# Optimization experiments

Hardware: AMD Instinct MI355X
Metric: run time of the kernel (lower is better)

Reference implementation:

```python
import jax, jax.numpy as jnp
import numpy as np

N = 100_000      # nodes
E = 3_200_000    # edges (avg degree 32)
F_IN, H, C = 1433, 16, 7


def setup_inputs() -> dict:
    key = jax.random.key(0)
    ks = jax.random.split(key, 8)
    x = jax.random.normal(ks[0], (N, F_IN), jnp.float32)
    edge_index = jax.random.randint(ks[1], (2, E), 0, N, dtype=jnp.int32)
    s_in = 1.0 / np.sqrt(F_IN)
    s_h = 1.0 / np.sqrt(H)
    w_root1 = jax.random.normal(ks[2], (F_IN, H), jnp.float32) * s_in
    w_rel1 = jax.random.normal(ks[3], (F_IN, H), jnp.float32) * s_in
    b_rel1 = jnp.zeros((H,), jnp.float32)
    w_root2 = jax.random.normal(ks[4], (H, C), jnp.float32) * s_h
    w_rel2 = jax.random.normal(ks[5], (H, C), jnp.float32) * s_h
    b_rel2 = jnp.zeros((C,), jnp.float32)
    return {"x": x, "edge_index": edge_index,
            "w_root1": w_root1, "w_rel1": w_rel1, "b_rel1": b_rel1,
            "w_root2": w_root2, "w_rel2": w_rel2, "b_rel2": b_rel2}


def _graph_conv(x, src, dst, w_root, w_rel, b_rel, n_nodes):
    # GraphConv: out_i = W_root x_i + W_rel * sum_{j->i} x_j + b.
    # Sum-aggregation commutes with the linear map, so project first
    # (avoids gathering full-width features per edge).
    h = x @ w_rel                                   # [N, out]
    agg = jax.ops.segment_sum(h[src], dst, num_segments=n_nodes)  # [N, out]
    return agg + b_rel + x @ w_root


def reference(x, edge_index, w_root1, w_rel1, b_rel1, w_root2, w_rel2, b_rel2):
    src, dst = edge_index[0], edge_index[1]
    h1 = jax.nn.elu(_graph_conv(x, src, dst, w_root1, w_rel1, b_rel1, N))
    # F.dropout(training=self.training) -> identity in eval mode
    h2 = _graph_conv(h1, src, dst, w_root2, w_rel2, b_rel2, N)
    return jax.nn.log_softmax(h2, axis=1)
```

## Files before the change

### kernel.cpp

```cpp
#include <hip/hip_runtime.h>
#include <hip/hip_bf16.h>
#include <math.h>

#define FIN  1433
#define HID  16
#define NCLS 7
#define BM   128
#define BK   32
#define KS   4
#define KT_TOTAL 45
#define KPAD (KT_TOTAL * BK)

typedef __attribute__((ext_vector_type(8))) short bf16x8;
typedef __attribute__((ext_vector_type(4))) float f32x4;

__global__ __launch_bounds__(256) void k_wt(
    const float* __restrict__ w_root, const float* __restrict__ w_rel,
    ushort* __restrict__ wT) {
  int idx = blockIdx.x * 256 + threadIdx.x;
  if (idx >= 32 * KPAD) return;
  int c = idx / KPAD, k = idx % KPAD;
  float v = 0.f;
  if (k < FIN) v = (c < HID) ? w_rel[k * HID + c] : w_root[k * HID + (c - HID)];
  __hip_bfloat16 h = __float2bfloat16(v);
  wT[idx] = *(ushort*)&h;
}

__global__ __launch_bounds__(256) void k1_mfma(
    const float* __restrict__ x, const ushort* __restrict__ wT,
    const float* __restrict__ b_rel,
    float* __restrict__ pbase, float* __restrict__ abase,
    size_t seg, int n) {
  __shared__ ushort xs[2][BM * BK];
  __shared__ ushort wsh[2][32 * BK];

  const int tid  = threadIdx.x;
  const int lane = tid & 63;
  const int wave = tid >> 6;
  const int row0 = blockIdx.x * BM;
  const int slice = blockIdx.y;
  const int kt_beg = (KT_TOTAL * slice) / KS;
  const int kt_end = (KT_TOTAL * (slice + 1)) / KS;

  f32x4 acc[2][2] = {};

  const int sr  = tid >> 5;
  const int sk  = tid & 31;
  const int wc  = tid >> 3;
  const int wt4 = tid & 7;

  float  xr[16];
  ushort4 wr;

  auto load_tile = [&](int kt) {
    const int k0 = kt * BK;
    const int gk = k0 + sk;
    const bool kv = gk < FIN;
#pragma unroll
    for (int i = 0; i < 16; ++i) {
      int gr = row0 + i * 8 + sr;
      xr[i] = (gr < n && kv) ? x[(size_t)gr * FIN + gk] : 0.f;
    }
    wr = *(const ushort4*)&wT[(size_t)wc * KPAD + k0 + wt4 * 4];
  };

  auto store_stage = [&](int b) {
#pragma unroll
    for (int i = 0; i < 16; ++i) {
      __hip_bfloat16 h = __float2bfloat16(xr[i]);
      xs[b][(i * 8 + sr) * BK + sk] = *(ushort*)&h;
    }
    *(ushort4*)&wsh[b][wc * BK + wt4 * 4] = wr;
  };

  const int m = lane & 15, o = lane >> 4;

  auto do_mfma = [&](int b) {
    bf16x8 b0 = *(const bf16x8*)&wsh[b][(m)      * BK + o * 8];
    bf16x8 b1 = *(const bf16x8*)&wsh[b][(16 + m) * BK + o * 8];
#pragma unroll
    for (int mf = 0; mf < 2; ++mf) {
      bf16x8 a = *(const bf16x8*)&xs[b][(wave * 32 + mf * 16 + m) * BK + o * 8];
      acc[mf][0] = __builtin_amdgcn_mfma_f32_16x16x32_bf16(a, b0, acc[mf][0], 0, 0, 0);
      acc[mf][1] = __builtin_amdgcn_mfma_f32_16x16x32_bf16(a, b1, acc[mf][1], 0, 0, 0);
    }
  };

  load_tile(kt_beg);
  store_stage(0);
  __syncthreads();
  for (int t = kt_beg; t < kt_end; ++t) {
    const int b = (t - kt_beg) & 1;
    const bool more = (t + 1) < kt_end;
    if (more) load_tile(t + 1);
    do_mfma(b);
    if (more) store_stage(b ^ 1);
    __syncthreads();
  }

  float* __restrict__ p_out = pbase + (size_t)slice * seg;
  float* __restrict__ a_out = abase + (size_t)slice * seg;
  const float bv = (slice == 0) ? b_rel[m] : 0.f;
#pragma unroll
  for (int mf = 0; mf < 2; ++mf) {
#pragma unroll
    for (int j = 0; j < 4; ++j) {
      int gr = row0 + wave * 32 + mf * 16 + o * 4 + j;
      if (gr < n) {
        p_out[(size_t)gr * HID + m] = acc[mf][0][j];
        a_out[(size_t)gr * HID + m] = acc[mf][1][j] + bv;
      }
    }
  }
}

__global__ __launch_bounds__(256) void k_reduce(
    float* __restrict__ pbase, float* __restrict__ abase,
    size_t seg_elems, int n4) {
  int i = blockIdx.x * 256 + threadIdx.x;
  if (i >= n4) return;
  size_t s4 = seg_elems / 4;
  float4 a = ((const float4*)pbase)[i];
  float4 c = ((const float4*)abase)[i];
#pragma unroll
  for (int s = 1; s < KS; ++s) {
    float4 b = ((const float4*)pbase)[i + s * s4];
    float4 d = ((const float4*)abase)[i + s * s4];
    a.x += b.x; a.y += b.y; a.z += b.z; a.w += b.w;
    c.x += d.x; c.y += d.y; c.z += d.z; c.w += d.w;
  }
  ((float4*)pbase)[i] = a;
  ((float4*)abase)[i] = c;
}

__global__ __launch_bounds__(256) void k2_scatter16(
    const int* __restrict__ ei, const float* __restrict__ p,
    float* __restrict__ agg, int nE) {
  long long tid = (long long)blockIdx.x * 256 + threadIdx.x;
  if (tid >= (long long)nE * HID) return;
  int e = (int)(tid >> 4), f = (int)(tid & 15);
  int s = ei[e], d = ei[nE + e];
  unsafeAtomicAdd(agg + (size_t)d * HID + f, p[(size_t)s * HID + f]);
}

__global__ __launch_bounds__(256) void k3_l2(
    const float* __restrict__ agg,
    const float* __restrict__ w_root2, const float* __restrict__ w_rel2,
    const float* __restrict__ b2,
    float* __restrict__ p2, float* __restrict__ out2, int n) {
  int i = blockIdx.x * 256 + threadIdx.x;
  if (i >= n) return;
  const float4* a4 = (const float4*)(agg + (size_t)i * HID);
  float h[HID];
#pragma unroll
  for (int q = 0; q < 4; ++q) {
    float4 v = a4[q];
    float t[4] = {v.x, v.y, v.z, v.w};
#pragma unroll
    for (int j = 0; j < 4; ++j)
      h[4*q + j] = t[j] > 0.f ? t[j] : expm1f(t[j]);
  }
#pragma unroll
  for (int c = 0; c < NCLS; ++c) {
    float sr = 0.f, so = b2[c];
#pragma unroll
    for (int k = 0; k < HID; ++k) {
      sr = fmaf(h[k], w_rel2[k * NCLS + c], sr);
      so = fmaf(h[k], w_root2[k * NCLS + c], so);
    }
    p2[(size_t)i * NCLS + c] = sr;
    out2[(size_t)i * NCLS + c] = so;
  }
}

__global__ __launch_bounds__(256) void k4_scatter7(
    const int* __restrict__ ei, const float* __restrict__ p,
    float* __restrict__ out2, int nE) {
  long long tid = (long long)blockIdx.x * 256 + threadIdx.x;
  int e = (int)(tid >> 3), f = (int)(tid & 7);
  if (e >= nE || f >= NCLS) return;
  int s = ei[e], d = ei[nE + e];
  unsafeAtomicAdd(out2 + (size_t)d * NCLS + f, p[(size_t)s * NCLS + f]);
}

__global__ __launch_bounds__(256) void k5_lsm(float* __restrict__ out, int n) {
  int i = blockIdx.x * 256 + threadIdx.x;
  if (i >= n) return;
  float v[NCLS];
  float* o = out + (size_t)i * NCLS;
#pragma unroll
  for (int c = 0; c < NCLS; ++c) v[c] = o[c];
  float m = v[0];
#pragma unroll
  for (int c = 1; c < NCLS; ++c) m = fmaxf(m, v[c]);
  float s = 0.f;
#pragma unroll
  for (int c = 0; c < NCLS; ++c) s += expf(v[c] - m);
  float l = logf(s);
#pragma unroll
  for (int c = 0; c < NCLS; ++c) o[c] = v[c] - m - l;
}

extern "C" void kernel_launch(void* const* d_in, const int* in_sizes, int n_in,
                              void* d_out, int out_size, void* d_ws, size_t ws_size,
                              hipStream_t stream) {
  const float* x       = (const float*)d_in[0];
  const int*   ei      = (const int*)  d_in[1];
  const float* w_root1 = (const float*)d_in[2];
  const float* w_rel1  = (const float*)d_in[3];
  const float* b_rel1  = (const float*)d_in[4];
  const float* w_root2 = (const float*)d_in[5];
  const float* w_rel2  = (const float*)d_in[6];
  const float* b_rel2  = (const float*)d_in[7];
  float* out = (float*)d_out;

  int n  = in_sizes[0] / FIN;
  int nE = in_sizes[1] / 2;

  size_t seg = (size_t)n * HID;
  char* ws = (char*)d_ws;
  float*  pbase = (float*)ws;
  float*  abase = pbase + KS * seg;
  float*  p2    = abase + KS * seg;
  ushort* wT    = (ushort*)(p2 + (size_t)n * NCLS);

  int nbN = (n + 255) / 256;

  k_wt<<<(32 * KPAD + 255) / 256, 256, 0, stream>>>(w_root1, w_rel1, wT);

  dim3 g1((n + BM - 1) / BM, KS);
  k1_mfma<<<g1, 256, 0, stream>>>(x, wT, b_rel1, pbase, abase, seg, n);
  int n4 = n * HID / 4;
  k_reduce<<<(n4 + 255) / 256, 256, 0, stream>>>(pbase, abase, seg, n4);

  long long t2 = (long long)nE * HID;
  k2_scatter16<<<(int)((t2 + 255) / 256), 256, 0, stream>>>(ei, pbase, abase, nE);

  k3_l2<<<nbN, 256, 0, stream>>>(abase, w_root2, w_rel2, b_rel2, p2, out, n);
  long long t4 = (long long)nE * 8;
  k4_scatter7<<<(int)((t4 + 255) / 256), 256, 0, stream>>>(ei, p2, out, nE);

  k5_lsm<<<nbN, 256, 0, stream>>>(out, n);
}
```

Baseline: 555.9 us.

## Store intermediates in bf16 and scatter with packed bf16 atomics

Split-K partials, aggregation buffers and layer-2 projections are now kept in bf16 instead of fp32. Both edge scatters use global_atomic_pk_add_bf16, so each atomic adds two features and half as many atomics are issued. Layer-2 rows are padded to 8 bf16 values for aligned 16-byte loads and stores. The aim is to halve atomic count and memory traffic in the scatter-heavy phases, at the cost of bf16 rounding in sums over many edges, which may hurt accuracy.

```diff
diff --git a/kernel.cpp b/kernel.cpp
--- a/kernel.cpp
+++ b/kernel.cpp
@@ -14,6 +14,19 @@
 typedef __attribute__((ext_vector_type(8))) short bf16x8;
 typedef __attribute__((ext_vector_type(4))) float f32x4;
 
+__device__ inline float bf2f(ushort u) {
+  unsigned int t = ((unsigned int)u) << 16;
+  return __uint_as_float(t);
+}
+__device__ inline ushort f2bf(float f) {
+  __hip_bfloat16 h = __float2bfloat16(f);
+  return *(ushort*)&h;
+}
+__device__ inline void pk_atomic_bf16(void* addr, unsigned int data) {
+  asm volatile("global_atomic_pk_add_bf16 %0, %1, off"
+               :: "v"((unsigned long long)addr), "v"(data) : "memory");
+}
+
 __global__ __launch_bounds__(256) void k_wt(
     const float* __restrict__ w_root, const float* __restrict__ w_rel,
     ushort* __restrict__ wT) {
@@ -22,14 +35,13 @@
   int c = idx / KPAD, k = idx % KPAD;
   float v = 0.f;
   if (k < FIN) v = (c < HID) ? w_rel[k * HID + c] : w_root[k * HID + (c - HID)];
-  __hip_bfloat16 h = __float2bfloat16(v);
-  wT[idx] = *(ushort*)&h;
+  wT[idx] = f2bf(v);
 }
 
 __global__ __launch_bounds__(256) void k1_mfma(
     const float* __restrict__ x, const ushort* __restrict__ wT,
     const float* __restrict__ b_rel,
-    float* __restrict__ pbase, float* __restrict__ abase,
+    ushort* __restrict__ pbase, ushort* __restrict__ abase,
     size_t seg, int n) {
   __shared__ ushort xs[2][BM * BK];
   __shared__ ushort wsh[2][32 * BK];
@@ -66,10 +78,8 @@
 
   auto store_stage = [&](int b) {
 #pragma unroll
-    for (int i = 0; i < 16; ++i) {
-      __hip_bfloat16 h = __float2bfloat16(xr[i]);
-      xs[b][(i * 8 + sr) * BK + sk] = *(ushort*)&h;
-    }
+    for (int i = 0; i < 16; ++i)
+      xs[b][(i * 8 + sr) * BK + sk] = f2bf(xr[i]);
     *(ushort4*)&wsh[b][wc * BK + wt4 * 4] = wr;
   };
 
@@ -98,8 +108,8 @@
     __syncthreads();
   }
 
-  float* __restrict__ p_out = pbase + (size_t)slice * seg;
-  float* __restrict__ a_out = abase + (size_t)slice * seg;
+  ushort* __restrict__ p_out = pbase + (size_t)slice * seg;
+  ushort* __restrict__ a_out = abase + (size_t)slice * seg;
   const float bv = (slice == 0) ? b_rel[m] : 0.f;
 #pragma unroll
   for (int mf = 0; mf < 2; ++mf) {
@@ -107,89 +117,127 @@
     for (int j = 0; j < 4; ++j) {
       int gr = row0 + wave * 32 + mf * 16 + o * 4 + j;
       if (gr < n) {
-        p_out[(size_t)gr * HID + m] = acc[mf][0][j];
-        a_out[(size_t)gr * HID + m] = acc[mf][1][j] + bv;
+        p_out[(size_t)gr * HID + m] = f2bf(acc[mf][0][j]);
+        a_out[(size_t)gr * HID + m] = f2bf(acc[mf][1][j] + bv);
       }
     }
   }
 }
 
 __global__ __launch_bounds__(256) void k_reduce(
-    float* __restrict__ pbase, float* __restrict__ abase,
-    size_t seg_elems, int n4) {
+    ushort* __restrict__ pbase, ushort* __restrict__ abase,
+    size_t seg, int n8) {
   int i = blockIdx.x * 256 + threadIdx.x;
-  if (i >= n4) return;
-  size_t s4 = seg_elems / 4;
-  float4 a = ((const float4*)pbase)[i];
-  float4 c = ((const float4*)abase)[i];
-#pragma unroll
-  for (int s = 1; s < KS; ++s) {
-    float4 b = ((const float4*)pbase)[i + s * s4];
-    float4 d = ((const float4*)abase)[i + s * s4];
-    a.x += b.x; a.y += b.y; a.z += b.z; a.w += b.w;
-    c.x += d.x; c.y += d.y; c.z += d.z; c.w += d.w;
-  }
-  ((float4*)pbase)[i] = a;
-  ((float4*)abase)[i] = c;
-}
-
-__global__ __launch_bounds__(256) void k2_scatter16(
-    const int* __restrict__ ei, const float* __restrict__ p,
-    float* __restrict__ agg, int nE) {
+  if (i >= n8) return;
+  float ps[8], as[8];
+#pragma unroll
+  for (int j = 0; j < 8; ++j) { ps[j] = 0.f; as[j] = 0.f; }
+#pragma unroll
+  for (int s = 0; s < KS; ++s) {
+    uint4 pv = ((const uint4*)(pbase + s * seg))[i];
+    uint4 av = ((const uint4*)(abase + s * seg))[i];
+    const unsigned int pw[4] = {pv.x, pv.y, pv.z, pv.w};
+    const unsigned int aw[4] = {av.x, av.y, av.z, av.w};
+#pragma unroll
+    for (int q = 0; q < 4; ++q) {
+      ps[2*q]   += bf2f((ushort)(pw[q] & 0xffff));
+      ps[2*q+1] += bf2f((ushort)(pw[q] >> 16));
+      as[2*q]   += bf2f((ushort)(aw[q] & 0xffff));
+      as[2*q+1] += bf2f((ushort)(aw[q] >> 16));
+    }
+  }
+  uint4 po, ao;
+  unsigned int* pw = (unsigned int*)&po;
+  unsigned int* aw = (unsigned int*)&ao;
+#pragma unroll
+  for (int q = 0; q < 4; ++q) {
+    pw[q] = (unsigned int)f2bf(ps[2*q]) | ((unsigned int)f2bf(ps[2*q+1]) << 16);
+    aw[q] = (unsigned int)f2bf(as[2*q]) | ((unsigned int)f2bf(as[2*q+1]) << 16);
+  }
+  ((uint4*)pbase)[i] = po;
+  ((uint4*)abase)[i] = ao;
+}
+
+__global__ __launch_bounds__(256) void k2_scatter(
+    const int* __restrict__ ei, const ushort* __restrict__ p1,
+    ushort* __restrict__ agg, int nE) {
   long long tid = (long long)blockIdx.x * 256 + threadIdx.x;
-  if (tid >= (long long)nE * HID) return;
-  int e = (int)(tid >> 4), f = (int)(tid & 15);
+  if (tid >= (long long)nE * 8) return;
+  int e = (int)(tid >> 3), f = (int)(tid & 7);
   int s = ei[e], d = ei[nE + e];
-  unsafeAtomicAdd(agg + (size_t)d * HID + f, p[(size_t)s * HID + f]);
+  unsigned int v = ((const unsigned int*)p1)[(size_t)s * 8 + f];
+  pk_atomic_bf16((unsigned int*)agg + (size_t)d * 8 + f, v);
 }
 
 __global__ __launch_bounds__(256) void k3_l2(
-    const float* __restrict__ agg,
+    const ushort* __restrict__ agg,
     const float* __restrict__ w_root2, const float* __restrict__ w_rel2,
     const float* __restrict__ b2,
-    float* __restrict__ p2, float* __restrict__ out2, int n) {
+    ushort* __restrict__ p2, ushort* __restrict__ out_bf, int n) {
   int i = blockIdx.x * 256 + threadIdx.x;
   if (i >= n) return;
-  const float4* a4 = (const float4*)(agg + (size_t)i * HID);
   float h[HID];
+  const uint4* arow = (const uint4*)(agg + (size_t)i * HID);
+#pragma unroll
+  for (int half = 0; half < 2; ++half) {
+    uint4 v = arow[half];
+    const unsigned int w[4] = {v.x, v.y, v.z, v.w};
+#pragma unroll
+    for (int q = 0; q < 4; ++q) {
+      float t0 = bf2f((ushort)(w[q] & 0xffff));
+      float t1 = bf2f((ushort)(w[q] >> 16));
+      h[half*8 + 2*q]     = t0 > 0.f ? t0 : expm1f(t0);
+      h[half*8 + 2*q + 1] = t1 > 0.f ? t1 : expm1f(t1);
+    }
+  }
+  float sr[8], so[8];
+#pragma unroll
+  for (int c = 0; c < 8; ++c) { sr[c] = 0.f; so[c] = 0.f; }
+#pragma unroll
+  for (int c = 0; c < NCLS; ++c) {
+    float a = 0.f, b = b2[c];
+#pragma unroll
+    for (int k = 0; k < HID; ++k) {
+      a = fmaf(h[k], w_rel2[k * NCLS + c], a);
+      b = fmaf(h[k], w_root2[k * NCLS + c], b);
+    }
+    sr[c] = a; so[c] = b;
+  }
+  uint4 pv, ov;
+  unsigned int* pw = (unsigned int*)&pv;
+  unsigned int* ow = (unsigned int*)&ov;
 #pragma unroll
   for (int q = 0; q < 4; ++q) {
-    float4 v = a4[q];
-    float t[4] = {v.x, v.y, v.z, v.w};
-#pragma unroll
-    for (int j = 0; j < 4; ++j)
-      h[4*q + j] = t[j] > 0.f ? t[j] : expm1f(t[j]);
-  }
-#pragma unroll
-  for (int c = 0; c < NCLS; ++c) {
-    float sr = 0.f, so = b2[c];
-#pragma unroll
-    for (int k = 0; k < HID; ++k) {
-      sr = fmaf(h[k], w_rel2[k * NCLS + c], sr);
-      so = fmaf(h[k], w_root2[k * NCLS + c], so);
-    }
-    p2[(size_t)i * NCLS + c] = sr;
-    out2[(size_t)i * NCLS + c] = so;
-  }
-}
-
-__global__ __launch_bounds__(256) void k4_scatter7(
-    const int* __restrict__ ei, const float* __restrict__ p,
-    float* __restrict__ out2, int nE) {
+    pw[q] = (unsigned int)f2bf(sr[2*q]) | ((unsigned int)f2bf(sr[2*q+1]) << 16);
+    ow[q] = (unsigned int)f2bf(so[2*q]) | ((unsigned int)f2bf(so[2*q+1]) << 16);
+  }
+  ((uint4*)(p2     + (size_t)i * 8))[0] = pv;
+  ((uint4*)(out_bf + (size_t)i * 8))[0] = ov;
+}
+
+__global__ __launch_bounds__(256) void k4_scatter(
+    const int* __restrict__ ei, const ushort* __restrict__ p2,
+    ushort* __restrict__ out_bf, int nE) {
   long long tid = (long long)blockIdx.x * 256 + threadIdx.x;
-  int e = (int)(tid >> 3), f = (int)(tid & 7);
-  if (e >= nE || f >= NCLS) return;
+  if (tid >= (long long)nE * 4) return;
+  int e = (int)(tid >> 2), f = (int)(tid & 3);
   int s = ei[e], d = ei[nE + e];
-  unsafeAtomicAdd(out2 + (size_t)d * NCLS + f, p[(size_t)s * NCLS + f]);
-}
-
-__global__ __launch_bounds__(256) void k5_lsm(float* __restrict__ out, int n) {
+  unsigned int v = ((const unsigned int*)p2)[(size_t)s * 4 + f];
+  pk_atomic_bf16((unsigned int*)out_bf + (size_t)d * 4 + f, v);
+}
+
+__global__ __launch_bounds__(256) void k5_lsm(
+    const ushort* __restrict__ out_bf, float* __restrict__ out, int n) {
   int i = blockIdx.x * 256 + threadIdx.x;
   if (i >= n) return;
-  float v[NCLS];
-  float* o = out + (size_t)i * NCLS;
-#pragma unroll
-  for (int c = 0; c < NCLS; ++c) v[c] = o[c];
+  uint4 rv = ((const uint4*)(out_bf + (size_t)i * 8))[0];
+  const unsigned int w[4] = {rv.x, rv.y, rv.z, rv.w};
+  float v[8];
+#pragma unroll
+  for (int q = 0; q < 4; ++q) {
+    v[2*q]   = bf2f((ushort)(w[q] & 0xffff));
+    v[2*q+1] = bf2f((ushort)(w[q] >> 16));
+  }
   float m = v[0];
 #pragma unroll
   for (int c = 1; c < NCLS; ++c) m = fmaxf(m, v[c]);
@@ -197,6 +245,7 @@
 #pragma unroll
   for (int c = 0; c < NCLS; ++c) s += expf(v[c] - m);
   float l = logf(s);
+  float* o = out + (size_t)i * NCLS;
 #pragma unroll
   for (int c = 0; c < NCLS; ++c) o[c] = v[c] - m - l;
 }
@@ -219,10 +268,11 @@
 
   size_t seg = (size_t)n * HID;
   char* ws = (char*)d_ws;
-  float*  pbase = (float*)ws;
-  float*  abase = pbase + KS * seg;
-  float*  p2    = abase + KS * seg;
-  ushort* wT    = (ushort*)(p2 + (size_t)n * NCLS);
+  ushort* pbase = (ushort*)ws;
+  ushort* abase = pbase + KS * seg;
+  ushort* p2    = abase + KS * seg;
+  ushort* outbf = p2 + (size_t)n * 8;
+  ushort* wT    = outbf + (size_t)n * 8;
 
   int nbN = (n + 255) / 256;
 
@@ -230,15 +280,16 @@
 
   dim3 g1((n + BM - 1) / BM, KS);
   k1_mfma<<<g1, 256, 0, stream>>>(x, wT, b_rel1, pbase, abase, seg, n);
-  int n4 = n * HID / 4;
-  k_reduce<<<(n4 + 255) / 256, 256, 0, stream>>>(pbase, abase, seg, n4);
-
-  long long t2 = (long long)nE * HID;
-  k2_scatter16<<<(int)((t2 + 255) / 256), 256, 0, stream>>>(ei, pbase, abase, nE);
-
-  k3_l2<<<nbN, 256, 0, stream>>>(abase, w_root2, w_rel2, b_rel2, p2, out, n);
-  long long t4 = (long long)nE * 8;
-  k4_scatter7<<<(int)((t4 + 255) / 256), 256, 0, stream>>>(ei, p2, out, nE);
-
-  k5_lsm<<<nbN, 256, 0, stream>>>(out, n);
-}
+  int n8 = n * HID / 8;
+  k_reduce<<<(n8 + 255) / 256, 256, 0, stream>>>(pbase, abase, seg, n8);
+
+  long long t2 = (long long)nE * 8;
+  k2_scatter<<<(int)((t2 + 255) / 256), 256, 0, stream>>>(ei, pbase, abase, nE);
+
+  k3_l2<<<nbN, 256, 0, stream>>>(abase, w_root2, w_rel2, b_rel2, p2, outbf, n);
+
+  long long t4 = (long long)nE * 4;
+  k4_scatter<<<(int)((t4 + 255) / 256), 256, 0, stream>>>(ei, p2, outbf, nE);
+
+  k5_lsm<<<nbN, 256, 0, stream>>>(outbf, out, n);
+}
```

New measurement: 479.8 us. -13.7%, faster.
